# Performance work log

Hardware: AMD Instinct MI355X
Metric: run time of the kernel (lower is better)

Reference implementation:

```python
import jax, jax.numpy as jnp
import numpy as np

K = 4        # maximum_fertility + 1
OOV_ID = 1
HIDDEN = 512


def setup_inputs() -> dict:
    key = jax.random.key(0)
    ks = jax.random.split(key, 8)
    B, S, D, E, H, V = 4, 128, 512, 256, HIDDEN, 32000
    return {
        "embedded_input": jax.random.normal(ks[0], (B, S, D), jnp.float32),
        "input_mask": jnp.ones((B, S), jnp.int32),
        "emb_table": jax.random.normal(ks[1], (V, E), jnp.float32) * 0.02,
        "W_ih": jax.random.normal(ks[2], (4 * H, D + E), jnp.float32) * 0.02,
        "b_ih": jax.random.normal(ks[3], (4 * H,), jnp.float32) * 0.02,
        "W_hh": jax.random.normal(ks[4], (4 * H, H), jnp.float32) * 0.02,
        "b_hh": jax.random.normal(ks[5], (4 * H,), jnp.float32) * 0.02,
        "W_out": jax.random.normal(ks[6], (V, H), jnp.float32) * 0.02,
        "b_out": jax.random.normal(ks[7], (V,), jnp.float32) * 0.02,
    }


def reference(embedded_input, input_mask, emb_table, W_ih, b_ih, W_hh, b_hh, W_out, b_out):
    B, S, D = embedded_input.shape
    V, E = emb_table.shape
    H = HIDDEN
    N = B * S
    x = embedded_input.reshape(N, D)                      # (N, D)
    h0 = jnp.zeros((N, H), embedded_input.dtype)
    c0 = jnp.zeros((N, H), embedded_input.dtype)
    # initial last_output: one-hot at OOV id (prob mass 1.0 on oov)
    last0 = jnp.zeros((N, V), embedded_input.dtype).at[:, OOV_ID].set(1.0)

    def step(carry, _):
        h, c, last = carry
        # embedding_bag soft mix over full vocab == weighted sum == matmul
        emb_last = last @ emb_table                        # (N, E)
        inp = jnp.concatenate([x, emb_last], axis=1)       # (N, D+E)
        gates = inp @ W_ih.T + b_ih + h @ W_hh.T + b_hh    # (N, 4H)
        i, f, g, o = jnp.split(gates, 4, axis=1)           # torch LSTMCell gate order
        i = jax.nn.sigmoid(i)
        f = jax.nn.sigmoid(f)
        g = jnp.tanh(g)
        o = jax.nn.sigmoid(o)
        c_new = f * c + i * g
        h_new = o * jnp.tanh(c_new)
        # dropout=0 / eval -> dropout mask is all ones (no-op)
        logits = h_new @ W_out.T + b_out                   # (N, V)
        logp = jax.nn.log_softmax(logits, axis=-1)
        return (h_new, c_new, jnp.exp(logp)), logp

    _, outs = jax.lax.scan(step, (h0, c0, last0), None, length=K)  # (K, N, V)
    return outs.transpose(1, 0, 2).reshape(B, S, K, V)
```

## Files before the change

### kernel.cpp

```cpp
#include <hip/hip_runtime.h>
#include <hip/hip_bf16.h>
#include <math.h>

#define N_ROWS 512
#define D_IN   512
#define E_EMB  256
#define H_DIM  512
#define G_DIM  2048
#define V_DIM  32000
#define IN_LD  1280
#define K_STEPS 4
#define OOV_ID 1
#define TBK 64
#define EMB_SPLIT 25
#define EMB_CHUNK 1280
#define SEGSTRIDE 512

typedef __attribute__((ext_vector_type(4))) float f32x4;
typedef __attribute__((ext_vector_type(8))) short bf16x8;

__device__ inline short f2b(float v) {
    __hip_bfloat16 h = __float2bfloat16(v);
    return *reinterpret_cast<short*>(&h);
}

__device__ inline void gload_lds(const short* g, short* l) {
    __builtin_amdgcn_global_load_lds(
        (const __attribute__((address_space(1))) void*)g,
        (__attribute__((address_space(3))) void*)l, 16, 0, 0);
}

template<int TBM, int TBN, int MODE, int STATS>
__global__ __launch_bounds__(256) void k_gemm(
    const short* __restrict__ A, int lda,
    const short* __restrict__ B, int ldb,
    const float* __restrict__ bias,
    float* __restrict__ C, size_t ldc, int Kc,
    float2* __restrict__ stats)
{
    constexpr int WMT = TBM / 2, WNT = TBN / 2;
    constexpr int WM = WMT / 16, WN = WNT / 16;
    __shared__ short As[TBM * 64];
    __shared__ short Bs[TBN * 64];
    const int tid = threadIdx.x;
    const int lane = tid & 63, wid = tid >> 6;
    const int wr = wid & 1, wc = wid >> 1;
    const int quad = lane >> 4, l16 = lane & 15;
    const int m0 = blockIdx.y * TBM, n0 = blockIdx.x * TBN;
    const int kbase = blockIdx.z * Kc;
    const int lrow = lane >> 3;
    const int lsw  = ((lane & 7) ^ lrow) * 8;

    f32x4 acc[WM][WN];
#pragma unroll
    for (int i = 0; i < WM; ++i)
#pragma unroll
        for (int j = 0; j < WN; ++j)
#pragma unroll
            for (int r = 0; r < 4; ++r) acc[i][j][r] = 0.0f;

    for (int kt = 0; kt < Kc; kt += TBK) {
        const int k0 = kbase + kt;
#pragma unroll
        for (int ch = wid; ch < TBM / 8; ch += 4)
            gload_lds(&A[(size_t)(m0 + ch * 8 + lrow) * lda + k0 + lsw], &As[ch * 512]);
#pragma unroll
        for (int ch = wid; ch < TBN / 8; ch += 4)
            gload_lds(&B[(size_t)(n0 + ch * 8 + lrow) * ldb + k0 + lsw], &Bs[ch * 512]);
        __syncthreads();
#pragma unroll
        for (int ks = 0; ks < 2; ++ks) {
            bf16x8 af[WM], bfv[WN];
#pragma unroll
            for (int i = 0; i < WM; ++i) {
                int rr = wr * WMT + i * 16 + l16;
                af[i] = *(const bf16x8*)&As[rr * 64 + (((ks * 4 + quad) ^ (l16 & 7)) * 8)];
            }
#pragma unroll
            for (int j = 0; j < WN; ++j) {
                int rr = wc * WNT + j * 16 + l16;
                bfv[j] = *(const bf16x8*)&Bs[rr * 64 + (((ks * 4 + quad) ^ (l16 & 7)) * 8)];
            }
#pragma unroll
            for (int i = 0; i < WM; ++i)
#pragma unroll
                for (int j = 0; j < WN; ++j)
                    acc[i][j] = __builtin_amdgcn_mfma_f32_16x16x32_bf16(af[i], bfv[j], acc[i][j], 0, 0, 0);
        }
        __syncthreads();
    }

    if (MODE == 1) {
#pragma unroll
        for (int i = 0; i < WM; ++i)
#pragma unroll
            for (int j = 0; j < WN; ++j) {
                const int n = n0 + wc * WNT + j * 16 + l16;
#pragma unroll
                for (int r = 0; r < 4; ++r) {
                    const int m = m0 + wr * WMT + i * 16 + quad * 4 + r;
                    atomicAdd(&C[(size_t)m * ldc + n], acc[i][j][r]);
                }
            }
    } else {
        float bv[WN];
#pragma unroll
        for (int j = 0; j < WN; ++j) bv[j] = bias[n0 + wc * WNT + j * 16 + l16];
#pragma unroll
        for (int i = 0; i < WM; ++i) {
            if (!STATS) {
#pragma unroll
                for (int j = 0; j < WN; ++j) {
                    const int n = n0 + wc * WNT + j * 16 + l16;
#pragma unroll
                    for (int r = 0; r < 4; ++r) {
                        const int m = m0 + wr * WMT + i * 16 + quad * 4 + r;
                        C[(size_t)m * ldc + n] = acc[i][j][r] + bv[j];
                    }
                }
            } else {
                float rm[4] = {-1e30f, -1e30f, -1e30f, -1e30f};
                float rs[4] = {0.f, 0.f, 0.f, 0.f};
#pragma unroll
                for (int j = 0; j < WN; ++j)
#pragma unroll
                    for (int r = 0; r < 4; ++r)
                        rm[r] = fmaxf(rm[r], acc[i][j][r] + bv[j]);
#pragma unroll
                for (int j = 0; j < WN; ++j) {
                    const int n = n0 + wc * WNT + j * 16 + l16;
#pragma unroll
                    for (int r = 0; r < 4; ++r) {
                        const int m = m0 + wr * WMT + i * 16 + quad * 4 + r;
                        float z = acc[i][j][r] + bv[j];
                        rs[r] += __expf(z - rm[r]);
                        C[(size_t)m * ldc + n] = z;
                    }
                }
#pragma unroll
                for (int mask = 1; mask < 16; mask <<= 1) {
#pragma unroll
                    for (int r = 0; r < 4; ++r) {
                        float om = __shfl_xor(rm[r], mask);
                        float os = __shfl_xor(rs[r], mask);
                        float nm = fmaxf(rm[r], om);
                        rs[r] = rs[r] * __expf(rm[r] - nm) + os * __expf(om - nm);
                        rm[r] = nm;
                    }
                }
                if (l16 == 0) {
                    const int seg = blockIdx.x * 2 + wc;
#pragma unroll
                    for (int r = 0; r < 4; ++r) {
                        const int m = m0 + wr * WMT + i * 16 + quad * 4 + r;
                        stats[(size_t)m * SEGSTRIDE + seg] = make_float2(rm[r], rs[r]);
                    }
                }
            }
        }
    }
}

__global__ __launch_bounds__(256) void k_prep(
    const float* __restrict__ x, const float* __restrict__ emb_table,
    const float* __restrict__ W_ih, const float* __restrict__ W_hh,
    const float* __restrict__ b_ih, const float* __restrict__ b_hh,
    const float* __restrict__ W_out,
    short* __restrict__ Abuf, short* __restrict__ Wg, float* __restrict__ bsum,
    short* __restrict__ Wout16, float* __restrict__ c)
{
    const int idx0 = blockIdx.x * 256 + threadIdx.x;
    const int gs = gridDim.x * 256;
    const float4* W4 = (const float4*)W_out;
    for (int i = idx0; i < V_DIM * H_DIM / 4; i += gs) {
        float4 v = W4[i];
        short4 o;
        o.x = f2b(v.x); o.y = f2b(v.y); o.z = f2b(v.z); o.w = f2b(v.w);
        ((short4*)Wout16)[i] = o;
    }
    for (int i = idx0; i < G_DIM * IN_LD; i += gs) {
        int g = i / IN_LD, k = i - g * IN_LD;
        float v = (k < D_IN + E_EMB) ? W_ih[(size_t)g * (D_IN + E_EMB) + k]
                                     : W_hh[(size_t)g * H_DIM + (k - (D_IN + E_EMB))];
        Wg[i] = f2b(v);
    }
    for (int i = idx0; i < G_DIM; i += gs) bsum[i] = b_ih[i] + b_hh[i];
    for (int i = idx0; i < N_ROWS * IN_LD; i += gs) {
        int n = i / IN_LD, col = i - n * IN_LD;
        float v;
        if (col < D_IN)              v = x[(size_t)n * D_IN + col];
        else if (col < D_IN + E_EMB) v = emb_table[(size_t)OOV_ID * E_EMB + (col - D_IN)];
        else                         v = 0.0f;
        Abuf[i] = f2b(v);
    }
    for (int i = idx0; i < N_ROWS * H_DIM; i += gs) c[i] = 0.0f;
}

__global__ __launch_bounds__(256) void k_trans(const float* __restrict__ emb,
                                               short* __restrict__ embT)
{
    __shared__ float tile[64][65];
    const int v0 = blockIdx.x * 64, e0 = blockIdx.y * 64;
    const int tid = threadIdx.x;
#pragma unroll
    for (int i = 0; i < 16; ++i) {
        int idx = tid + i * 256;
        int vr = idx >> 6, ec = idx & 63;
        tile[vr][ec] = emb[(size_t)(v0 + vr) * E_EMB + e0 + ec];
    }
    __syncthreads();
#pragma unroll
    for (int i = 0; i < 16; ++i) {
        int idx = tid + i * 256;
        int er = idx >> 6, vc = idx & 63;
        embT[(size_t)(e0 + er) * V_DIM + v0 + vc] = f2b(tile[vc][er]);
    }
}

__global__ __launch_bounds__(256) void k_lstm(const float* __restrict__ gates,
                                              float* __restrict__ c,
                                              short* __restrict__ Abuf)
{
    int idx = blockIdx.x * blockDim.x + threadIdx.x;
    if (idx >= N_ROWS * H_DIM) return;
    int n = idx / H_DIM, j = idx - n * H_DIM;
    const float* gr = gates + (size_t)n * G_DIM;
    float gi = gr[j], gf = gr[j + H_DIM], gg = gr[j + 2 * H_DIM], go = gr[j + 3 * H_DIM];
    float i_ = 1.0f / (1.0f + expf(-gi));
    float f_ = 1.0f / (1.0f + expf(-gf));
    float g_ = tanhf(gg);
    float o_ = 1.0f / (1.0f + expf(-go));
    float cn = f_ * c[idx] + i_ * g_;
    float hn = o_ * tanhf(cn);
    c[idx] = cn;
    Abuf[(size_t)n * IN_LD + (D_IN + E_EMB) + j] = f2b(hn);
}

__global__ __launch_bounds__(256) void k_cvt_emb(const float* __restrict__ emb_acc,
                                                 short* __restrict__ Abuf)
{
    int idx = blockIdx.x * 256 + threadIdx.x;
    int n = idx >> 8, e = idx & 255;
    Abuf[(size_t)n * IN_LD + D_IN + e] = f2b(emb_acc[idx]);
}

__global__ __launch_bounds__(256) void k_lse(const float2* __restrict__ stats,
                                             float* __restrict__ lse,
                                             float* __restrict__ emb_acc,
                                             int feed)
{
    const int tid = threadIdx.x;
    const int lane = tid & 63, wid = tid >> 6;
    const int n = blockIdx.x * 4 + wid;

    float m = -1e30f, s = 0.0f;
    for (int sg = lane; sg < V_DIM / 64; sg += 64) {
        float2 p = stats[(size_t)n * SEGSTRIDE + sg];
        float nm = fmaxf(m, p.x);
        s = s * __expf(m - nm) + p.y * __expf(p.x - nm);
        m = nm;
    }
#pragma unroll
    for (int mask = 32; mask > 0; mask >>= 1) {
        float om = __shfl_xor(m, mask);
        float os = __shfl_xor(s, mask);
        float nm = fmaxf(m, om);
        s = s * __expf(m - nm) + os * __expf(om - nm);
        m = nm;
    }
    if (lane == 0) lse[n] = m + __logf(s);

    if (feed) {
        ((float4*)&emb_acc[(size_t)n * E_EMB])[lane] = make_float4(0.f, 0.f, 0.f, 0.f);
    }
}

__global__ __launch_bounds__(256) void k_finish(float* __restrict__ out,
                                                short* __restrict__ last,
                                                const float* __restrict__ lse,
                                                int step, int feed)
{
    const int n = blockIdx.y;
    const float l = lse[n];
    float4* row4 = (float4*)(out + ((size_t)n * K_STEPS + step) * V_DIM);
    short4* prow = (short4*)(last + (size_t)n * V_DIM);
    const int c0 = blockIdx.x * 1024 + threadIdx.x;
#pragma unroll
    for (int i = 0; i < 4; ++i) {
        const int c = c0 + i * 256;
        if (c < V_DIM / 4) {
            float4 xv = row4[c];
            xv.x -= l; xv.y -= l; xv.z -= l; xv.w -= l;
            row4[c] = xv;
            if (feed) {
                short4 p;
                p.x = f2b(__expf(xv.x)); p.y = f2b(__expf(xv.y));
                p.z = f2b(__expf(xv.z)); p.w = f2b(__expf(xv.w));
                prow[c] = p;
            }
        }
    }
}

extern "C" void kernel_launch(void* const* d_in, const int* in_sizes, int n_in,
                              void* d_out, int out_size, void* d_ws, size_t ws_size,
                              hipStream_t stream) {
    (void)in_sizes; (void)n_in; (void)out_size; (void)ws_size;
    const float* x       = (const float*)d_in[0];
    const float* emb_tab = (const float*)d_in[2];
    const float* W_ih    = (const float*)d_in[3];
    const float* b_ih    = (const float*)d_in[4];
    const float* W_hh    = (const float*)d_in[5];
    const float* b_hh    = (const float*)d_in[6];
    const float* W_out   = (const float*)d_in[7];
    const float* b_out   = (const float*)d_in[8];
    float* out = (float*)d_out;

    char* ws = (char*)d_ws;
    short* Abuf   = (short*)ws;  ws += (size_t)N_ROWS * IN_LD * sizeof(short);
    float* c      = (float*)ws;  ws += (size_t)N_ROWS * H_DIM * sizeof(float);
    float* gates  = (float*)ws;  ws += (size_t)N_ROWS * G_DIM * sizeof(float);
    short* last   = (short*)ws;  ws += (size_t)N_ROWS * V_DIM * sizeof(short);
    short* Wout16 = (short*)ws;  ws += (size_t)V_DIM * H_DIM * sizeof(short);
    short* Wg     = (short*)ws;  ws += (size_t)G_DIM * IN_LD * sizeof(short);
    float* bsum   = (float*)ws;  ws += (size_t)G_DIM * sizeof(float);
    short* embT   = (short*)ws;  ws += (size_t)E_EMB * V_DIM * sizeof(short);
    float* emb_acc= (float*)ws;  ws += (size_t)N_ROWS * E_EMB * sizeof(float);
    float2* stats = (float2*)ws; ws += (size_t)N_ROWS * SEGSTRIDE * sizeof(float2);
    float* lse    = (float*)ws;  ws += (size_t)N_ROWS * sizeof(float);

    k_prep<<<2048, 256, 0, stream>>>(x, emb_tab, W_ih, W_hh, b_ih, b_hh, W_out,
                                     Abuf, Wg, bsum, Wout16, c);
    k_trans<<<dim3(V_DIM / 64, E_EMB / 64), 256, 0, stream>>>(emb_tab, embT);

    for (int t = 0; t < K_STEPS; ++t) {
        if (t > 0) {
            k_gemm<128, 128, 1, 0><<<dim3(E_EMB / 128, N_ROWS / 128, EMB_SPLIT), 256, 0, stream>>>(
                last, V_DIM, embT, V_DIM, nullptr, emb_acc, E_EMB, EMB_CHUNK, nullptr);
            k_cvt_emb<<<N_ROWS * E_EMB / 256, 256, 0, stream>>>(emb_acc, Abuf);
        }
        k_gemm<64, 64, 0, 0><<<dim3(G_DIM / 64, N_ROWS / 64, 1), 256, 0, stream>>>(
            Abuf, IN_LD, Wg, IN_LD, bsum, gates, G_DIM, IN_LD, nullptr);
        k_lstm<<<(N_ROWS * H_DIM + 255) / 256, 256, 0, stream>>>(gates, c, Abuf);
        k_gemm<128, 128, 0, 1><<<dim3(V_DIM / 128, N_ROWS / 128, 1), 256, 0, stream>>>(
            Abuf + (D_IN + E_EMB), IN_LD, Wout16, H_DIM, b_out,
            out + (size_t)t * V_DIM, (size_t)K_STEPS * V_DIM, H_DIM, stats);
        const int feed = (t < K_STEPS - 1) ? 1 : 0;
        k_lse<<<N_ROWS / 4, 256, 0, stream>>>(stats, lse, emb_acc, feed);
        k_finish<<<dim3(8, N_ROWS), 256, 0, stream>>>(out, last, lse, t, feed);
    }
}
```

Measured before the change: 786.5 us.

## Fuse LSTM cell into gate GEMM epilogue and retile vocab and embedding GEMMs

Gate weight rows are permuted so each 64-column GEMM tile holds the i,f,g,o gates for the same 16 hidden units. The LSTM cell update then runs directly in the gate GEMM epilogue, which removes the separate k_lstm kernel and the fp32 gates buffer round trip. The GEMM template also gains configurable warp layouts: the vocab projection uses 256x128 tiles with 8 warps, and the embedding GEMM uses 128x256 tiles with 8 warps. Larger tiles cut redundant loads but reduce the number of blocks in flight.

After: 768.9 us. 2.2% less time.

```diff
diff --git a/kernel.cpp b/kernel.cpp
--- a/kernel.cpp
+++ b/kernel.cpp
@@ -30,21 +30,23 @@
         (__attribute__((address_space(3))) void*)l, 16, 0, 0);
 }
 
-template<int TBM, int TBN, int MODE, int STATS>
-__global__ __launch_bounds__(256) void k_gemm(
+template<int TBM, int TBN, int WR_, int WC_, int MODE, int STATS>
+__global__ __launch_bounds__(WR_ * WC_ * 64) void k_gemm(
     const short* __restrict__ A, int lda,
     const short* __restrict__ B, int ldb,
     const float* __restrict__ bias,
     float* __restrict__ C, size_t ldc, int Kc,
-    float2* __restrict__ stats)
-{
-    constexpr int WMT = TBM / 2, WNT = TBN / 2;
+    float2* __restrict__ stats,
+    float* __restrict__ cstate, short* __restrict__ hdst)
+{
+    constexpr int NW = WR_ * WC_;
+    constexpr int WMT = TBM / WR_, WNT = TBN / WC_;
     constexpr int WM = WMT / 16, WN = WNT / 16;
     __shared__ short As[TBM * 64];
     __shared__ short Bs[TBN * 64];
     const int tid = threadIdx.x;
     const int lane = tid & 63, wid = tid >> 6;
-    const int wr = wid & 1, wc = wid >> 1;
+    const int wr = wid % WR_, wc = wid / WR_;
     const int quad = lane >> 4, l16 = lane & 15;
     const int m0 = blockIdx.y * TBM, n0 = blockIdx.x * TBN;
     const int kbase = blockIdx.z * Kc;
@@ -62,10 +64,10 @@
     for (int kt = 0; kt < Kc; kt += TBK) {
         const int k0 = kbase + kt;
 #pragma unroll
-        for (int ch = wid; ch < TBM / 8; ch += 4)
+        for (int ch = wid; ch < TBM / 8; ch += NW)
             gload_lds(&A[(size_t)(m0 + ch * 8 + lrow) * lda + k0 + lsw], &As[ch * 512]);
 #pragma unroll
-        for (int ch = wid; ch < TBN / 8; ch += 4)
+        for (int ch = wid; ch < TBN / 8; ch += NW)
             gload_lds(&B[(size_t)(n0 + ch * 8 + lrow) * ldb + k0 + lsw], &Bs[ch * 512]);
         __syncthreads();
 #pragma unroll
@@ -90,7 +92,7 @@
         __syncthreads();
     }
 
-    if (MODE == 1) {
+    if constexpr (MODE == 1) {
 #pragma unroll
         for (int i = 0; i < WM; ++i)
 #pragma unroll
@@ -102,13 +104,37 @@
                     atomicAdd(&C[(size_t)m * ldc + n], acc[i][j][r]);
                 }
             }
+    } else if constexpr (MODE == 2) {
+        float bv[WN];
+#pragma unroll
+        for (int j = 0; j < WN; ++j) bv[j] = bias[n0 + j * 16 + l16];
+        const int jj = (n0 >> 2) + l16;
+#pragma unroll
+        for (int i = 0; i < WM; ++i) {
+#pragma unroll
+            for (int r = 0; r < 4; ++r) {
+                const int m = m0 + wr * WMT + i * 16 + quad * 4 + r;
+                float gi = acc[i][0][r] + bv[0];
+                float gf = acc[i][1][r] + bv[1];
+                float gg = acc[i][2][r] + bv[2];
+                float go = acc[i][3][r] + bv[3];
+                float i_ = 1.0f / (1.0f + expf(-gi));
+                float f_ = 1.0f / (1.0f + expf(-gf));
+                float g_ = tanhf(gg);
+                float o_ = 1.0f / (1.0f + expf(-go));
+                const size_t ci = (size_t)m * H_DIM + jj;
+                float cn = f_ * cstate[ci] + i_ * g_;
+                cstate[ci] = cn;
+                hdst[(size_t)m * IN_LD + (D_IN + E_EMB) + jj] = f2b(o_ * tanhf(cn));
+            }
+        }
     } else {
         float bv[WN];
 #pragma unroll
         for (int j = 0; j < WN; ++j) bv[j] = bias[n0 + wc * WNT + j * 16 + l16];
 #pragma unroll
         for (int i = 0; i < WM; ++i) {
-            if (!STATS) {
+            if constexpr (!STATS) {
 #pragma unroll
                 for (int j = 0; j < WN; ++j) {
                     const int n = n0 + wc * WNT + j * 16 + l16;
@@ -149,7 +175,7 @@
                     }
                 }
                 if (l16 == 0) {
-                    const int seg = blockIdx.x * 2 + wc;
+                    const int seg = (n0 + wc * WNT) >> 6;
 #pragma unroll
                     for (int r = 0; r < 4; ++r) {
                         const int m = m0 + wr * WMT + i * 16 + quad * 4 + r;
@@ -179,12 +205,20 @@
         ((short4*)Wout16)[i] = o;
     }
     for (int i = idx0; i < G_DIM * IN_LD; i += gs) {
-        int g = i / IN_LD, k = i - g * IN_LD;
+        int rp = i / IN_LD, k = i - rp * IN_LD;
+        int j = ((rp >> 6) << 4) | (rp & 15);
+        int gate = (rp >> 4) & 3;
+        int g = gate * H_DIM + j;
         float v = (k < D_IN + E_EMB) ? W_ih[(size_t)g * (D_IN + E_EMB) + k]
                                      : W_hh[(size_t)g * H_DIM + (k - (D_IN + E_EMB))];
         Wg[i] = f2b(v);
     }
-    for (int i = idx0; i < G_DIM; i += gs) bsum[i] = b_ih[i] + b_hh[i];
+    for (int i = idx0; i < G_DIM; i += gs) {
+        int j = ((i >> 6) << 4) | (i & 15);
+        int gate = (i >> 4) & 3;
+        int g = gate * H_DIM + j;
+        bsum[i] = b_ih[g] + b_hh[g];
+    }
     for (int i = idx0; i < N_ROWS * IN_LD; i += gs) {
         int n = i / IN_LD, col = i - n * IN_LD;
         float v;
@@ -215,25 +249,6 @@
         int er = idx >> 6, vc = idx & 63;
         embT[(size_t)(e0 + er) * V_DIM + v0 + vc] = f2b(tile[vc][er]);
     }
-}
-
-__global__ __launch_bounds__(256) void k_lstm(const float* __restrict__ gates,
-                                              float* __restrict__ c,
-                                              short* __restrict__ Abuf)
-{
-    int idx = blockIdx.x * blockDim.x + threadIdx.x;
-    if (idx >= N_ROWS * H_DIM) return;
-    int n = idx / H_DIM, j = idx - n * H_DIM;
-    const float* gr = gates + (size_t)n * G_DIM;
-    float gi = gr[j], gf = gr[j + H_DIM], gg = gr[j + 2 * H_DIM], go = gr[j + 3 * H_DIM];
-    float i_ = 1.0f / (1.0f + expf(-gi));
-    float f_ = 1.0f / (1.0f + expf(-gf));
-    float g_ = tanhf(gg);
-    float o_ = 1.0f / (1.0f + expf(-go));
-    float cn = f_ * c[idx] + i_ * g_;
-    float hn = o_ * tanhf(cn);
-    c[idx] = cn;
-    Abuf[(size_t)n * IN_LD + (D_IN + E_EMB) + j] = f2b(hn);
 }
 
 __global__ __launch_bounds__(256) void k_cvt_emb(const float* __restrict__ emb_acc,
@@ -319,7 +334,6 @@
     char* ws = (char*)d_ws;
     short* Abuf   = (short*)ws;  ws += (size_t)N_ROWS * IN_LD * sizeof(short);
     float* c      = (float*)ws;  ws += (size_t)N_ROWS * H_DIM * sizeof(float);
-    float* gates  = (float*)ws;  ws += (size_t)N_ROWS * G_DIM * sizeof(float);
     short* last   = (short*)ws;  ws += (size_t)N_ROWS * V_DIM * sizeof(short);
     short* Wout16 = (short*)ws;  ws += (size_t)V_DIM * H_DIM * sizeof(short);
     short* Wg     = (short*)ws;  ws += (size_t)G_DIM * IN_LD * sizeof(short);
@@ -335,16 +349,17 @@
 
     for (int t = 0; t < K_STEPS; ++t) {
         if (t > 0) {
-            k_gemm<128, 128, 1, 0><<<dim3(E_EMB / 128, N_ROWS / 128, EMB_SPLIT), 256, 0, stream>>>(
-                last, V_DIM, embT, V_DIM, nullptr, emb_acc, E_EMB, EMB_CHUNK, nullptr);
+            k_gemm<128, 256, 2, 4, 1, 0><<<dim3(1, N_ROWS / 128, EMB_SPLIT), 512, 0, stream>>>(
+                last, V_DIM, embT, V_DIM, nullptr, emb_acc, E_EMB, EMB_CHUNK,
+                nullptr, nullptr, nullptr);
             k_cvt_emb<<<N_ROWS * E_EMB / 256, 256, 0, stream>>>(emb_acc, Abuf);
         }
-        k_gemm<64, 64, 0, 0><<<dim3(G_DIM / 64, N_ROWS / 64, 1), 256, 0, stream>>>(
-            Abuf, IN_LD, Wg, IN_LD, bsum, gates, G_DIM, IN_LD, nullptr);
-        k_lstm<<<(N_ROWS * H_DIM + 255) / 256, 256, 0, stream>>>(gates, c, Abuf);
-        k_gemm<128, 128, 0, 1><<<dim3(V_DIM / 128, N_ROWS / 128, 1), 256, 0, stream>>>(
+        k_gemm<64, 64, 4, 1, 2, 0><<<dim3(G_DIM / 64, N_ROWS / 64, 1), 256, 0, stream>>>(
+            Abuf, IN_LD, Wg, IN_LD, bsum, nullptr, 0, IN_LD, nullptr, c, Abuf);
+        k_gemm<256, 128, 4, 2, 0, 1><<<dim3(V_DIM / 128, N_ROWS / 256, 1), 512, 0, stream>>>(
             Abuf + (D_IN + E_EMB), IN_LD, Wout16, H_DIM, b_out,
-            out + (size_t)t * V_DIM, (size_t)K_STEPS * V_DIM, H_DIM, stats);
+            out + (size_t)t * V_DIM, (size_t)K_STEPS * V_DIM, H_DIM, stats,
+            nullptr, nullptr);
         const int feed = (t < K_STEPS - 1) ? 1 : 0;
         k_lse<<<N_ROWS / 4, 256, 0, stream>>>(stats, lse, emb_acc, feed);
         k_finish<<<dim3(8, N_ROWS), 256, 0, stream>>>(out, last, lse, t, feed);
```
